# Optimization experiments

Measured on AMD Instinct MI355X. Metric: run time of the kernel, lower is better.

Reference implementation:

```python
import jax, jax.numpy as jnp
import numpy as np

B, C, E, HLR, WLR = 2, 64, 4, 192, 192


def setup_inputs() -> dict:
    key = jax.random.key(0)
    ks = jax.random.split(key, 8)
    s = 0.05  # keep activations/offsets in a sane range
    return {
        "x": jax.random.normal(ks[0], (B, C, HLR, WLR), jnp.float32),
        "fused": jax.random.normal(ks[1], (B, C, HLR, WLR), jnp.float32),
        "weight_compress": jax.random.normal(ks[2], (E, C // 8, C), jnp.float32) * s,
        "weight_expand": jax.random.normal(ks[3], (E, C, C // 8), jnp.float32) * s,
        "body_w1": jax.random.normal(ks[4], (64, 4), jnp.float32) * s,
        "body_b1": jnp.zeros((64,), jnp.float32),
        "body_w2": jax.random.normal(ks[5], (64, 64), jnp.float32) * s,
        "body_b2": jnp.zeros((64,), jnp.float32),
        "routing_w": jax.random.normal(ks[6], (E, 64), jnp.float32) * s,
        "routing_b": jnp.zeros((E,), jnp.float32),
        "offset_w": jax.random.normal(ks[7], (2, 64), jnp.float32) * s,
        "offset_b": jnp.zeros((2,), jnp.float32),
        "scale": 2,
    }


def _conv1x1(x, w, b):
    # x: [n, cin, H, W], w: [cout, cin] (1x1 conv)
    return jnp.einsum('oc,nchw->nohw', w, x) + b[None, :, None, None]


def _grid_sample(img, px, py):
    # Bilinear sample, align_corners=True semantics, zeros padding.
    # img: [b,c,h,w]; px, py: [b,H,W] absolute LR pixel coords.
    b, c, h, w = img.shape
    x0 = jnp.floor(px)
    y0 = jnp.floor(py)
    wx = (px - x0)[:, None]  # [b,1,H,W]
    wy = (py - y0)[:, None]

    def gather(xi, yi):
        valid = (xi >= 0) & (xi <= w - 1) & (yi >= 0) & (yi <= h - 1)
        xc = jnp.clip(xi, 0, w - 1).astype(jnp.int32)
        yc = jnp.clip(yi, 0, h - 1).astype(jnp.int32)
        v = jax.vmap(lambda im, yy, xx: im[:, yy, xx])(img, yc, xc)  # [b,c,H,W]
        return v * valid[:, None].astype(img.dtype)

    v00 = gather(x0, y0)
    v01 = gather(x0 + 1, y0)
    v10 = gather(x0, y0 + 1)
    v11 = gather(x0 + 1, y0 + 1)
    top = v00 * (1 - wx) + v01 * wx
    bot = v10 * (1 - wx) + v11 * wx
    return top * (1 - wy) + bot * wy


def reference(x, fused, weight_compress, weight_expand, body_w1, body_b1,
              body_w2, body_b2, routing_w, routing_b, offset_w, offset_b, scale):
    b, c, h, w = fused.shape
    H, W = round(h * scale), round(w * scale)
    e, c8 = weight_compress.shape[0], weight_compress.shape[1]

    ch = jnp.arange(H, dtype=jnp.float32)
    cw = jnp.arange(W, dtype=jnp.float32)
    coor_h = (ch + 0.5) / scale - jnp.floor((ch + 0.5) / scale + 0.001) - 0.5  # [H]
    coor_w = (cw + 0.5) / scale - jnp.floor((cw + 0.5) / scale + 0.001) - 0.5  # [W]
    inp = jnp.stack([
        jnp.full((H, W), 1.0 / scale, jnp.float32),
        jnp.full((H, W), 1.0 / scale, jnp.float32),
        jnp.broadcast_to(coor_h[:, None], (H, W)),
        jnp.broadcast_to(coor_w[None, :], (H, W)),
    ], 0)[None]  # [1,4,H,W]

    emb = jax.nn.relu(_conv1x1(inp, body_w1, body_b1))
    emb = jax.nn.relu(_conv1x1(emb, body_w2, body_b2))
    offset = _conv1x1(emb, offset_w, offset_b)            # [1,2,H,W]
    routing = jax.nn.sigmoid(_conv1x1(emb, routing_w, routing_b))  # [1,E,H,W]

    rw = routing.reshape(e, H * W).T                      # [HW, E]
    wc = (rw @ weight_compress.reshape(e, -1)).reshape(H, W, c8, c)  # per-pixel compress
    we = (rw @ weight_expand.reshape(e, -1)).reshape(H, W, c, c8)    # per-pixel expand

    # deformable sample: HR grid projected into LR space + learned offset (pixel units)
    px = jnp.broadcast_to((cw[None, :] + 0.5) / scale - 0.5, (H, W))[None] + offset[:, 0]
    py = jnp.broadcast_to((ch[:, None] + 0.5) / scale - 0.5, (H, W))[None] + offset[:, 1]
    px = jnp.broadcast_to(px, (b, H, W))
    py = jnp.broadcast_to(py, (b, H, W))
    fea0 = _grid_sample(fused, px, py)                    # [b,c,H,W]

    fea = fea0.transpose(0, 2, 3, 1)                      # [b,H,W,c]
    mid = jnp.einsum('hwoc,bhwc->bhwo', wc, fea)          # [b,H,W,c//8]
    out = jnp.einsum('hwco,bhwo->bhwc', we, mid)          # [b,H,W,c]
    return out.transpose(0, 3, 1, 2) + fea0
```

## Files before the change

### kernel.cpp

```cpp
#include <hip/hip_runtime.h>
#include <hip/hip_bf16.h>
#include <math.h>

typedef __attribute__((ext_vector_type(8))) short short8;
typedef __attribute__((ext_vector_type(4))) float f32x4;

#define HLR_ 192
#define WLR_ 192
#define H_ 384
#define W_ 384
#define LRP (HLR_*WLR_)
#define PTILES (LRP/64)
#define TPX 96
#define NTW (W_/TPX)
#define IPW 48

#define WS_K_OFF 4718592
#define WS_OFF_OFF (WS_K_OFF + 8192)

__device__ __forceinline__ unsigned short f32_bf16(float x){
    union { float f; unsigned int u; } v; v.f = x;
    unsigned int r = v.u + 0x7fffu + ((v.u >> 16) & 1u);
    return (unsigned short)(r >> 16);
}
__device__ __forceinline__ unsigned int pk_bf16(float a, float b){
    float2 t; t.x = a; t.y = b;
    __hip_bfloat162 h = __float22bfloat162_rn(t);
    union { __hip_bfloat162 h; unsigned int u; } c; c.h = h;
    return c.u;
}

__global__ __launch_bounds__(256) void prep_kernel(
    const float* __restrict__ fused, float* __restrict__ fused_t,
    const float* __restrict__ w1, const float* __restrict__ b1,
    const float* __restrict__ w2, const float* __restrict__ b2,
    const float* __restrict__ rw, const float* __restrict__ rb,
    const float* __restrict__ ow, const float* __restrict__ ob,
    const float* __restrict__ WC, const float* __restrict__ WE,
    unsigned short* __restrict__ Kmat, float* __restrict__ g_off)
{
    __shared__ float smem[8912];
    int bid = blockIdx.x;
    int tid = threadIdx.x;

    if (bid == 0) {
        float* sW2 = smem;
        float* sRW = smem + 4160;
        float* sE1 = smem + 4544;
        float* sR  = smem + 4800;
        float* sWc = smem + 4816;
        float* sWe = smem + 6864;

        for (int idx = tid; idx < 4096; idx += 256)
            sW2[(idx>>6)*65 + (idx&63)] = w2[idx];
        sRW[tid] = rw[tid];
        if (tid < 128) sRW[256 + tid] = ow[tid];

        int wave = tid >> 6, lane = tid & 63;
        int ph = wave >> 1, pw = wave & 1;

        float ch = (ph + 0.5f)*0.5f;
        float coor_h = ch - floorf(ch + 0.001f) - 0.5f;
        float cw = (pw + 0.5f)*0.5f;
        float coor_w = cw - floorf(cw + 0.001f) - 0.5f;

        float e1 = w1[lane*4+0]*0.5f + w1[lane*4+1]*0.5f
                 + w1[lane*4+2]*coor_h + w1[lane*4+3]*coor_w + b1[lane];
        sE1[wave*64 + lane] = fmaxf(e1, 0.0f);
        __syncthreads();

        float e2 = b2[lane];
        #pragma unroll 16
        for (int i = 0; i < 64; ++i) e2 += sW2[lane*65 + i] * sE1[wave*64 + i];
        e2 = fmaxf(e2, 0.0f);

        #pragma unroll
        for (int k = 0; k < 6; ++k) {
            float t = sRW[k*64 + lane] * e2;
            #pragma unroll
            for (int m = 1; m <= 32; m <<= 1) t += __shfl_xor(t, m, 64);
            if (lane == 0) {
                if (k < 4) sR[wave*4 + k] = 1.0f/(1.0f + expf(-(t + rb[k])));
                else       g_off[wave*2 + (k-4)] = t + ob[k-4];
            }
        }
        __syncthreads();

        for (int idx = tid; idx < 2048; idx += 256) {
            int cls = idx >> 9, rem = idx & 511;
            float r0=sR[cls*4+0], r1=sR[cls*4+1], r2=sR[cls*4+2], r3=sR[cls*4+3];
            sWc[cls*512 + rem] =
                r0*WC[0*512+rem] + r1*WC[1*512+rem] + r2*WC[2*512+rem] + r3*WC[3*512+rem];
        }
        for (int idx = tid; idx < 2048; idx += 256) {
            int cls = idx >> 9, rem = idx & 511;
            float r0=sR[cls*4+0], r1=sR[cls*4+1], r2=sR[cls*4+2], r3=sR[cls*4+3];
            sWe[cls*512 + rem] =
                r0*WE[0*512+rem] + r1*WE[1*512+rem] + r2*WE[2*512+rem] + r3*WE[3*512+rem];
        }
        __syncthreads();

        for (int idx = tid; idx < 16384; idx += 256) {
            int cls = idx >> 12, rem = idx & 4095;
            int c = rem >> 6, cp = rem & 63;
            float a = (c == cp) ? 1.0f : 0.0f;
            #pragma unroll
            for (int o = 0; o < 8; ++o)
                a += sWe[cls*512 + c*8 + o] * sWc[cls*512 + o*64 + cp];
            Kmat[idx] = f32_bf16(a);
        }
    } else {
        float* tile = smem;
        int id = bid - 1;
        int b = id / PTILES, pt = id % PTILES;
        int p0 = pt * 64;
        int tlo = tid & 63, thi = tid >> 6;
        #pragma unroll
        for (int i = 0; i < 16; ++i) {
            int c = thi + i*4;
            tile[c*65 + tlo] = fused[(size_t)(b*64 + c)*LRP + p0 + tlo];
        }
        __syncthreads();
        #pragma unroll
        for (int i = 0; i < 16; ++i) {
            int p = thi + i*4;
            fused_t[(size_t)(b*LRP + p0 + p)*64 + tlo] = tile[tlo*65 + p];
        }
    }
}

__global__ __launch_bounds__(256, 6) void main_kernel(
    const float* __restrict__ fused_t, const unsigned short* __restrict__ Kmat,
    const float* __restrict__ g_off, float* __restrict__ out)
{
    __shared__ unsigned short sFea[4*IPW*64];

    int g = blockIdx.x;
    int xcd = g & 7;
    int t = g >> 3;
    int q = t >> 2;
    int wt = t & 3;
    int h = xcd*48 + q;
    int w0 = wt * TPX;
    int tid = threadIdx.x, wave = tid >> 6, lane = tid & 63;
    int b = wave >> 1, par = wave & 1;
    int ph = h & 1, cls = ph*2 + par;

    float off0 = g_off[cls*2 + 0];
    float off1 = g_off[cls*2 + 1];

    float py  = (h + 0.5f)*0.5f - 0.5f + off1;
    float y0f = floorf(py);
    float wy  = py - y0f;
    int   y0  = (int)y0f;
    float fy0 = (y0 >= 0  && y0 <= HLR_-1) ? 1.0f : 0.0f;
    float fy1 = (y0 >= -1 && y0 <= HLR_-2) ? 1.0f : 0.0f;
    int   yc0 = min(max(y0, 0), HLR_-1);
    int   yc1 = min(max(y0+1, 0), HLR_-1);
    float omwy = 1.0f - wy;

    float pxb  = (w0 + par + 0.5f)*0.5f - 0.5f + off0;
    float x0bf = floorf(pxb);
    float wx   = pxb - x0bf;
    int   x0b  = (int)x0bf;
    float omwx = 1.0f - wx;

    float W00 = omwx*omwy*fy0, W01 = wx*omwy*fy0;
    float W10 = omwx*wy  *fy1, W11 = wx*wy  *fy1;

    int itg = lane >> 4;
    int cg  = lane & 15;

    const float* baseB = fused_t + (size_t)b * LRP * 64;
    const float* r0 = baseB + (size_t)yc0 * WLR_ * 64 + cg*4;
    const float* r1 = baseB + (size_t)yc1 * WLR_ * 64 + cg*4;
    unsigned short* sBaseW = sFea + ((wave*IPW) << 6) + (((cg & 1) << 2));
    int wchunk = cg >> 1;

    int xs = x0b + itg*12;
    int xc = min(max(xs, 0), WLR_-1);
    f32x4 p0 = *(const f32x4*)(r0 + (size_t)xc*64);
    f32x4 p1 = *(const f32x4*)(r1 + (size_t)xc*64);
    float fxp = (xs >= 0 && xs <= WLR_-1) ? 1.0f : 0.0f;

    #pragma unroll
    for (int j = 0; j < 12; ++j) {
        int xn = xs + j + 1;
        float fxn = (xn >= 0 && xn <= WLR_-1) ? 1.0f : 0.0f;
        int xcn = min(max(xn, 0), WLR_-1);
        f32x4 c0 = *(const f32x4*)(r0 + (size_t)xcn*64);
        f32x4 c1 = *(const f32x4*)(r1 + (size_t)xcn*64);
        float a00 = W00*fxp, a01 = W01*fxn, a10 = W10*fxp, a11 = W11*fxn;
        f32x4 v = p0*a00 + c0*a01 + p1*a10 + c1*a11;
        uint2 pv;
        pv.x = pk_bf16(v[0], v[1]);
        pv.y = pk_bf16(v[2], v[3]);
        int item = itg*12 + j;
        *(uint2*)(sBaseW + (item << 6) + (((wchunk ^ (item & 7)) << 3))) = pv;
        p0 = c0; p1 = c1; fxp = fxn;
    }
    __syncthreads();

    int lm = lane & 15, lg = lane >> 4;

    const unsigned short* Kc = Kmat + cls*4096;
    short8 Af[4][2];
    #pragma unroll
    for (int mt = 0; mt < 4; ++mt)
        #pragma unroll
        for (int kt = 0; kt < 2; ++kt)
            Af[mt][kt] = *(const short8*)(Kc + (mt*16 + lm)*64 + kt*32 + lg*8);

    #pragma unroll
    for (int nt = 0; nt < 3; ++nt) {
        int slot = nt*16 + lm;
        const unsigned short* sb = sFea + ((wave*IPW + slot) << 6);
        short8 B0 = *(const short8*)(sb + (((0*4 + lg) ^ (slot & 7)) << 3));
        short8 B1 = *(const short8*)(sb + (((1*4 + lg) ^ (slot & 7)) << 3));

        int wc = w0 + 2*slot + par;
        #pragma unroll
        for (int mt = 0; mt < 4; ++mt) {
            f32x4 a = {0.0f, 0.0f, 0.0f, 0.0f};
            a = __builtin_amdgcn_mfma_f32_16x16x32_bf16(Af[mt][0], B0, a, 0, 0, 0);
            a = __builtin_amdgcn_mfma_f32_16x16x32_bf16(Af[mt][1], B1, a, 0, 0, 0);
            int c0 = mt*16 + lg*4;
            float* op = out + (((size_t)(b*64 + c0)*H_ + h)*W_ + wc);
            op[0*(size_t)(H_*W_)] = a[0];
            op[1*(size_t)(H_*W_)] = a[1];
            op[2*(size_t)(H_*W_)] = a[2];
            op[3*(size_t)(H_*W_)] = a[3];
        }
    }
}

extern "C" void kernel_launch(void* const* d_in, const int* in_sizes, int n_in,
                              void* d_out, int out_size, void* d_ws, size_t ws_size,
                              hipStream_t stream)
{
    const float* fused = (const float*)d_in[1];
    const float* WC    = (const float*)d_in[2];
    const float* WE    = (const float*)d_in[3];
    const float* w1    = (const float*)d_in[4];
    const float* b1    = (const float*)d_in[5];
    const float* w2    = (const float*)d_in[6];
    const float* b2    = (const float*)d_in[7];
    const float* rw    = (const float*)d_in[8];
    const float* rb    = (const float*)d_in[9];
    const float* ow    = (const float*)d_in[10];
    const float* ob    = (const float*)d_in[11];
    (void)in_sizes; (void)n_in; (void)out_size; (void)ws_size;

    float* ws = (float*)d_ws;
    float* fused_t = ws;
    unsigned short* Kmat = (unsigned short*)(ws + WS_K_OFF);
    float* g_off = ws + WS_OFF_OFF;
    float* o = (float*)d_out;

    hipLaunchKernelGGL(prep_kernel, dim3(1 + 2*PTILES), dim3(256), 0, stream,
                       fused, fused_t, w1, b1, w2, b2, rw, rb, ow, ob, WC, WE,
                       Kmat, g_off);
    hipLaunchKernelGGL(main_kernel, dim3(H_*NTW), dim3(256), 0, stream,
                       fused_t, Kmat, g_off, o);
}
```

Baseline: 148.3 us.

## Store transposed features in fp16 and bilinear-interpolate in packed half math

The prep kernel now writes the channel-last copy of the LR feature map as fp16 instead of fp32, halving that intermediate buffer and the gather traffic in the main kernel. The main kernel loads 8 halves per lane, does bilinear interpolation with packed fp16 multiply-adds, and uses fp16 MFMA in place of bf16. The transpose load is also vectorized to 16-byte reads. Doing the interpolation in fp16 costs some accuracy, and the lane-to-item mapping and LDS swizzle change to match the new shape.

```diff
diff --git a/kernel.cpp b/kernel.cpp
--- a/kernel.cpp
+++ b/kernel.cpp
@@ -1,8 +1,8 @@
 #include <hip/hip_runtime.h>
-#include <hip/hip_bf16.h>
+#include <hip/hip_fp16.h>
 #include <math.h>
 
-typedef __attribute__((ext_vector_type(8))) short short8;
+typedef __attribute__((ext_vector_type(8))) _Float16 half8;
 typedef __attribute__((ext_vector_type(4))) float f32x4;
 
 #define HLR_ 192
@@ -14,24 +14,26 @@
 #define TPX 96
 #define NTW (W_/TPX)
 #define IPW 48
-
-#define WS_K_OFF 4718592
+#define RUN 6
+
+#define WS_K_OFF 2359296
 #define WS_OFF_OFF (WS_K_OFF + 8192)
 
-__device__ __forceinline__ unsigned short f32_bf16(float x){
-    union { float f; unsigned int u; } v; v.f = x;
-    unsigned int r = v.u + 0x7fffu + ((v.u >> 16) & 1u);
-    return (unsigned short)(r >> 16);
-}
-__device__ __forceinline__ unsigned int pk_bf16(float a, float b){
-    float2 t; t.x = a; t.y = b;
-    __hip_bfloat162 h = __float22bfloat162_rn(t);
-    union { __hip_bfloat162 h; unsigned int u; } c; c.h = h;
-    return c.u;
+__device__ __forceinline__ unsigned short f32_f16(float x){
+    union { _Float16 h; unsigned short u; } c; c.h = (_Float16)x; return c.u;
+}
+__device__ __forceinline__ unsigned int pk_f16(float a, float b){
+    union { _Float16 h[2]; unsigned int u; } c;
+    c.h[0] = (_Float16)a; c.h[1] = (_Float16)b; return c.u;
+}
+__device__ __forceinline__ half8 splat8(float f){
+    _Float16 h = (_Float16)f;
+    half8 v = {h,h,h,h,h,h,h,h};
+    return v;
 }
 
 __global__ __launch_bounds__(256) void prep_kernel(
-    const float* __restrict__ fused, float* __restrict__ fused_t,
+    const float* __restrict__ fused, unsigned short* __restrict__ fused_t,
     const float* __restrict__ w1, const float* __restrict__ b1,
     const float* __restrict__ w2, const float* __restrict__ b2,
     const float* __restrict__ rw, const float* __restrict__ rb,
@@ -107,30 +109,36 @@
             #pragma unroll
             for (int o = 0; o < 8; ++o)
                 a += sWe[cls*512 + c*8 + o] * sWc[cls*512 + o*64 + cp];
-            Kmat[idx] = f32_bf16(a);
+            Kmat[idx] = f32_f16(a);
         }
     } else {
         float* tile = smem;
         int id = bid - 1;
         int b = id / PTILES, pt = id % PTILES;
         int p0 = pt * 64;
-        int tlo = tid & 63, thi = tid >> 6;
-        #pragma unroll
-        for (int i = 0; i < 16; ++i) {
-            int c = thi + i*4;
-            tile[c*65 + tlo] = fused[(size_t)(b*64 + c)*LRP + p0 + tlo];
-        }
-        __syncthreads();
-        #pragma unroll
-        for (int i = 0; i < 16; ++i) {
-            int p = thi + i*4;
-            fused_t[(size_t)(b*LRP + p0 + p)*64 + tlo] = tile[tlo*65 + p];
+        #pragma unroll
+        for (int i = 0; i < 4; ++i) {
+            int n = tid + i*256;
+            int c = n >> 4, k = (n & 15) << 2;
+            f32x4 v = *(const f32x4*)(fused + (size_t)(b*64 + c)*LRP + p0 + k);
+            float* tp = tile + c*65 + k;
+            tp[0]=v[0]; tp[1]=v[1]; tp[2]=v[2]; tp[3]=v[3];
+        }
+        __syncthreads();
+        int c0 = (tid & 15) << 2, pr = tid >> 4;
+        #pragma unroll
+        for (int i = 0; i < 4; ++i) {
+            int p = pr + i*16;
+            uint2 pv;
+            pv.x = pk_f16(tile[(c0+0)*65 + p], tile[(c0+1)*65 + p]);
+            pv.y = pk_f16(tile[(c0+2)*65 + p], tile[(c0+3)*65 + p]);
+            *(uint2*)(fused_t + (((size_t)(b*LRP + p0 + p)) << 6) + c0) = pv;
         }
     }
 }
 
 __global__ __launch_bounds__(256, 6) void main_kernel(
-    const float* __restrict__ fused_t, const unsigned short* __restrict__ Kmat,
+    const unsigned short* __restrict__ fused_t, const unsigned short* __restrict__ Kmat,
     const float* __restrict__ g_off, float* __restrict__ out)
 {
     __shared__ unsigned short sFea[4*IPW*64];
@@ -168,35 +176,33 @@
     float W00 = omwx*omwy*fy0, W01 = wx*omwy*fy0;
     float W10 = omwx*wy  *fy1, W11 = wx*wy  *fy1;
 
-    int itg = lane >> 4;
-    int cg  = lane & 15;
-
-    const float* baseB = fused_t + (size_t)b * LRP * 64;
-    const float* r0 = baseB + (size_t)yc0 * WLR_ * 64 + cg*4;
-    const float* r1 = baseB + (size_t)yc1 * WLR_ * 64 + cg*4;
-    unsigned short* sBaseW = sFea + ((wave*IPW) << 6) + (((cg & 1) << 2));
-    int wchunk = cg >> 1;
-
-    int xs = x0b + itg*12;
+    int itg = lane >> 3;
+    int cg  = lane & 7;
+
+    const unsigned short* baseB = fused_t + (size_t)b * LRP * 64;
+    const unsigned short* r0 = baseB + (size_t)yc0 * WLR_ * 64 + cg*8;
+    const unsigned short* r1 = baseB + (size_t)yc1 * WLR_ * 64 + cg*8;
+    unsigned short* sW = sFea + wave*IPW*64;
+
+    int xs = x0b + itg*RUN;
     int xc = min(max(xs, 0), WLR_-1);
-    f32x4 p0 = *(const f32x4*)(r0 + (size_t)xc*64);
-    f32x4 p1 = *(const f32x4*)(r1 + (size_t)xc*64);
+    half8 p0 = *(const half8*)(r0 + (size_t)xc*64);
+    half8 p1 = *(const half8*)(r1 + (size_t)xc*64);
     float fxp = (xs >= 0 && xs <= WLR_-1) ? 1.0f : 0.0f;
 
     #pragma unroll
-    for (int j = 0; j < 12; ++j) {
+    for (int j = 0; j < RUN; ++j) {
         int xn = xs + j + 1;
         float fxn = (xn >= 0 && xn <= WLR_-1) ? 1.0f : 0.0f;
         int xcn = min(max(xn, 0), WLR_-1);
-        f32x4 c0 = *(const f32x4*)(r0 + (size_t)xcn*64);
-        f32x4 c1 = *(const f32x4*)(r1 + (size_t)xcn*64);
-        float a00 = W00*fxp, a01 = W01*fxn, a10 = W10*fxp, a11 = W11*fxn;
-        f32x4 v = p0*a00 + c0*a01 + p1*a10 + c1*a11;
-        uint2 pv;
-        pv.x = pk_bf16(v[0], v[1]);
-        pv.y = pk_bf16(v[2], v[3]);
-        int item = itg*12 + j;
-        *(uint2*)(sBaseW + (item << 6) + (((wchunk ^ (item & 7)) << 3))) = pv;
+        half8 c0 = *(const half8*)(r0 + (size_t)xcn*64);
+        half8 c1 = *(const half8*)(r1 + (size_t)xcn*64);
+        half8 v = p0*splat8(W00*fxp);
+        v += c0*splat8(W01*fxn);
+        v += p1*splat8(W10*fxp);
+        v += c1*splat8(W11*fxn);
+        int item = itg*RUN + j;
+        *(half8*)(sW + (item << 6) + ((cg ^ (item & 7)) << 3)) = v;
         p0 = c0; p1 = c1; fxp = fxn;
     }
     __syncthreads();
@@ -204,28 +210,28 @@
     int lm = lane & 15, lg = lane >> 4;
 
     const unsigned short* Kc = Kmat + cls*4096;
-    short8 Af[4][2];
+    half8 Af[4][2];
     #pragma unroll
     for (int mt = 0; mt < 4; ++mt)
         #pragma unroll
         for (int kt = 0; kt < 2; ++kt)
-            Af[mt][kt] = *(const short8*)(Kc + (mt*16 + lm)*64 + kt*32 + lg*8);
+            Af[mt][kt] = *(const half8*)(Kc + (mt*16 + lm)*64 + kt*32 + lg*8);
 
     #pragma unroll
     for (int nt = 0; nt < 3; ++nt) {
         int slot = nt*16 + lm;
-        const unsigned short* sb = sFea + ((wave*IPW + slot) << 6);
-        short8 B0 = *(const short8*)(sb + (((0*4 + lg) ^ (slot & 7)) << 3));
-        short8 B1 = *(const short8*)(sb + (((1*4 + lg) ^ (slot & 7)) << 3));
+        const unsigned short* sb = sFea + (wave*IPW + slot)*64;
+        half8 B0 = *(const half8*)(sb + (((0*4 + lg) ^ (slot & 7)) << 3));
+        half8 B1 = *(const half8*)(sb + (((1*4 + lg) ^ (slot & 7)) << 3));
 
         int wc = w0 + 2*slot + par;
         #pragma unroll
         for (int mt = 0; mt < 4; ++mt) {
             f32x4 a = {0.0f, 0.0f, 0.0f, 0.0f};
-            a = __builtin_amdgcn_mfma_f32_16x16x32_bf16(Af[mt][0], B0, a, 0, 0, 0);
-            a = __builtin_amdgcn_mfma_f32_16x16x32_bf16(Af[mt][1], B1, a, 0, 0, 0);
-            int c0 = mt*16 + lg*4;
-            float* op = out + (((size_t)(b*64 + c0)*H_ + h)*W_ + wc);
+            a = __builtin_amdgcn_mfma_f32_16x16x32_f16(Af[mt][0], B0, a, 0, 0, 0);
+            a = __builtin_amdgcn_mfma_f32_16x16x32_f16(Af[mt][1], B1, a, 0, 0, 0);
+            int c0r = mt*16 + lg*4;
+            float* op = out + (((size_t)(b*64 + c0r)*H_ + h)*W_ + wc);
             op[0*(size_t)(H_*W_)] = a[0];
             op[1*(size_t)(H_*W_)] = a[1];
             op[2*(size_t)(H_*W_)] = a[2];
@@ -252,7 +258,7 @@
     (void)in_sizes; (void)n_in; (void)out_size; (void)ws_size;
 
     float* ws = (float*)d_ws;
-    float* fused_t = ws;
+    unsigned short* fused_t = (unsigned short*)ws;
     unsigned short* Kmat = (unsigned short*)(ws + WS_K_OFF);
     float* g_off = ws + WS_OFF_OFF;
     float* o = (float*)d_out;
```

Result: faster. 144.0 us, median of 2 (-2.9%).
